# Kernel tuning notes

Hardware: AMD Instinct MI355X
Metric: run time of the kernel (lower is better)

Reference implementation:

```python
import jax, jax.numpy as jnp
import numpy as np

D_MODEL = 512
D_STATE = 16
D_CONV = 4
EXPAND = 2
D_INNER = EXPAND * D_MODEL  # 1024
DT_RANK = D_MODEL // 16     # 32 (ceil(512/16))
BATCH, SEQ = 8, 1024


def setup_inputs() -> dict:
    key = jax.random.key(0)
    ks = jax.random.split(key, 10)
    w = lambda i, shape, s=0.02: (jax.random.normal(ks[i], shape, jnp.float32) * s)
    return {
        "x": jax.random.normal(ks[0], (BATCH, SEQ, D_MODEL), jnp.float32),
        # Mamba params
        "W_in": w(1, (2 * D_INNER, D_MODEL)),            # in_proj (no bias)
        "conv_w": w(2, (D_INNER, D_CONV), 0.1),          # depthwise causal conv
        "conv_b": jnp.zeros((D_INNER,), jnp.float32),
        "W_x": w(3, (DT_RANK + 2 * D_STATE, D_INNER)),   # x_proj (no bias)
        "W_dt": w(4, (D_INNER, DT_RANK)),                # dt_proj
        "b_dt": jnp.full((D_INNER,), -4.6, jnp.float32), # -> softplus ~ 0.01
        "A_log": jnp.log(jnp.broadcast_to(
            jnp.arange(1, D_STATE + 1, dtype=jnp.float32), (D_INNER, D_STATE))),
        "D": jnp.ones((D_INNER,), jnp.float32),
        "W_out": w(5, (D_MODEL, D_INNER)),               # out_proj (no bias)
        # LayerNorm + head
        "ln_g": jnp.ones((D_MODEL,), jnp.float32),
        "ln_b": jnp.zeros((D_MODEL,), jnp.float32),
        "head_W": w(6, (D_MODEL, D_MODEL)),
        "head_b": jnp.zeros((D_MODEL,), jnp.float32),
    }


def reference(x, W_in, conv_w, conv_b, W_x, W_dt, b_dt, A_log, D, W_out,
              ln_g, ln_b, head_W, head_b):
    B, L, _ = x.shape
    # in_proj -> split into x branch and gate z
    xz = x @ W_in.T                               # (B, L, 2*D_INNER)
    xi, z = jnp.split(xz, 2, axis=-1)
    # causal depthwise conv1d over time (pad left d_conv-1), then SiLU
    xp = jnp.pad(xi, ((0, 0), (D_CONV - 1, 0), (0, 0)))
    xc = conv_b + sum(conv_w[:, k] * xp[:, k:k + L, :] for k in range(D_CONV))
    xc = jax.nn.silu(xc)                          # (B, L, D_INNER)
    # x_proj -> dt, B, C
    dbc = xc @ W_x.T
    dt = jax.nn.softplus(dbc[..., :DT_RANK] @ W_dt.T + b_dt)   # (B, L, D_INNER)
    Bm = dbc[..., DT_RANK:DT_RANK + D_STATE]                   # (B, L, D_STATE)
    Cm = dbc[..., DT_RANK + D_STATE:]                          # (B, L, D_STATE)
    A = -jnp.exp(A_log)                                        # (D_INNER, D_STATE)

    def step(h, ins):
        dt_t, B_t, C_t, u_t = ins                 # (B,Din) (B,Ds) (B,Ds) (B,Din)
        dA = jnp.exp(dt_t[:, :, None] * A)        # (B, Din, Ds)
        h = dA * h + (dt_t * u_t)[:, :, None] * B_t[:, None, :]
        y = jnp.einsum('bds,bs->bd', h, C_t)
        return h, y

    h0 = jnp.zeros((B, D_INNER, D_STATE), x.dtype)
    xs = (dt.transpose(1, 0, 2), Bm.transpose(1, 0, 2),
          Cm.transpose(1, 0, 2), xc.transpose(1, 0, 2))
    _, ys = jax.lax.scan(step, h0, xs)            # ys: (L, B, D_INNER)
    y = ys.transpose(1, 0, 2) + D * xc
    y = y * jax.nn.silu(z)
    out = y @ W_out.T                             # (B, L, D_MODEL)
    # LayerNorm is per-token, so norm the last token only (== LN(out)[:, -1])
    last = out[:, -1, :]
    mu = last.mean(-1, keepdims=True)
    var = ((last - mu) ** 2).mean(-1, keepdims=True)
    lastn = (last - mu) / jnp.sqrt(var + 1e-5) * ln_g + ln_b
    return lastn @ head_W.T + head_b              # (B, D_MODEL)
```

## Files before the change

kernel.cpp:

```cpp
#include <hip/hip_runtime.h>
#include <stdint.h>

#define B_   8
#define L_   1024
#define DM   512
#define DI   1024
#define DS   16
#define DTR  32
#define M_   (B_*L_)

typedef short v8s __attribute__((ext_vector_type(8)));
typedef short v4s __attribute__((ext_vector_type(4)));
typedef float v4f __attribute__((ext_vector_type(4)));

static __device__ __forceinline__ short f2bf(float f) {
  union { float f; uint32_t u; } v; v.f = f;
  uint32_t r = v.u + 0x7FFFu + ((v.u >> 16) & 1u);
  return (short)(r >> 16);
}
static __device__ __forceinline__ float bf2f(short s) {
  union { uint32_t u; float f; } v; v.u = ((uint32_t)(uint16_t)s) << 16; return v.f;
}
static __device__ __forceinline__ float silu_fast(float a) {
  return a * __builtin_amdgcn_rcpf(1.f + __expf(-a));
}
static __device__ __forceinline__ float wsum(float v) {
#pragma unroll
  for (int o = 32; o > 0; o >>= 1) v += __shfl_xor(v, o, 64);
  return v;
}
static __device__ __forceinline__ void gl_lds16(const short* g, short* l) {
  __builtin_amdgcn_global_load_lds(
      (const __attribute__((address_space(1))) void*)g,
      (__attribute__((address_space(3))) void*)l, 16, 0, 0);
}

__global__ __launch_bounds__(256) void k_prep(const float* __restrict__ x,
                                              const float* __restrict__ w_in,
                                              const float* __restrict__ w_x,
                                              const float* __restrict__ w_dt,
                                              const float* __restrict__ a_log,
                                              short* xb, short* wib, short* wxb, short* wdtb,
                                              float* Aneg, float* zlast) {
  if (blockIdx.x >= 4704) {
    int w = (int)(blockIdx.x - 4704) * 4 + (threadIdx.x >> 6);
    int l = threadIdx.x & 63;
    int b = w >> 10, j = w & 1023;
    const v4f* xr = (const v4f*)(x + ((size_t)(b * L_ + L_ - 1)) * DM);
    const v4f* wr = (const v4f*)(w_in + (size_t)(DI + j) * DM);
    float s = 0.f;
#pragma unroll
    for (int i = 0; i < 2; ++i) {
      v4f a = xr[l + 64 * i], c = wr[l + 64 * i];
      s += a[0]*c[0] + a[1]*c[1] + a[2]*c[2] + a[3]*c[3];
    }
    s = wsum(s);
    if (l == 0) zlast[b * DI + j] = s;
    return;
  }
  int idx = (blockIdx.x * 256 + threadIdx.x) * 4;
  const int n0 = M_ * DM, n1 = DI * DM, n2 = 48 * DI, n3 = DI * DTR, n4 = DI * DS;
  const float* src; short* dst;
  if (idx < n0)              { src = x + idx;    dst = xb + idx; }
  else if ((idx -= n0) < n1) { src = w_in + idx; dst = wib + idx; }
  else if ((idx -= n1) < n2) { src = w_x + idx;  dst = wxb + idx; }
  else if ((idx -= n2) < n3) { src = w_dt + idx; dst = wdtb + idx; }
  else if ((idx -= n3) < n4) {
    v4f v = *(const v4f*)(a_log + idx);
    v4f o;
#pragma unroll
    for (int i = 0; i < 4; ++i) o[i] = -__expf(v[i]);
    *(v4f*)(Aneg + idx) = o;
    return;
  }
  else return;
  v4f v = *(const v4f*)src;
  v4s o;
#pragma unroll
  for (int i = 0; i < 4; ++i) o[i] = f2bf(v[i]);
  *(v4s*)dst = o;
}

__global__ __launch_bounds__(256) void k_gemm_xi(const short* __restrict__ xb,
                                                 const short* __restrict__ wib,
                                                 short* __restrict__ xib) {
  __shared__ short sh[128 * 136];
  short* lA = sh;
  short* lB = sh + 128 * 64;
  int mb = blockIdx.x >> 3, nb = blockIdx.x & 7;
  int tid = threadIdx.x;
  int w = tid >> 6, l = tid & 63, lm = l & 15, q = l >> 4;
  int wm = (w >> 1) * 64, wn = (w & 1) * 64;

  v4f acc[4][4];
#pragma unroll
  for (int i = 0; i < 4; ++i)
#pragma unroll
    for (int j = 0; j < 4; ++j) acc[i][j] = (v4f){0,0,0,0};

  int srow_in_chunk = l >> 3;
  int sslot = l & 7;
  const short* Abase = xb  + (size_t)(mb * 128) * DM;
  const short* Bbase = wib + (size_t)(nb * 128) * DM;

  for (int k0 = 0; k0 < DM; k0 += 64) {
    if (k0) __syncthreads();
#pragma unroll
    for (int i = 0; i < 4; ++i) {
      int chunk = w * 4 + i;
      int row = chunk * 8 + srow_in_chunk;
      int c = sslot ^ (row & 7);
      gl_lds16(Abase + (size_t)row * DM + k0 + c * 8, lA + chunk * 512);
      gl_lds16(Bbase + (size_t)row * DM + k0 + c * 8, lB + chunk * 512);
    }
    __syncthreads();
#pragma unroll
    for (int kt = 0; kt < 2; ++kt) {
      v8s af[4], bf[4];
      int p = (kt * 4 + q) ^ (lm & 7);
#pragma unroll
      for (int t = 0; t < 4; ++t) {
        af[t] = *(const v8s*)(lA + (wm + t * 16 + lm) * 64 + p * 8);
        bf[t] = *(const v8s*)(lB + (wn + t * 16 + lm) * 64 + p * 8);
      }
#pragma unroll
      for (int i = 0; i < 4; ++i)
#pragma unroll
        for (int j = 0; j < 4; ++j)
          acc[i][j] = __builtin_amdgcn_mfma_f32_16x16x32_bf16(af[i], bf[j], acc[i][j], 0, 0, 0);
    }
  }
  __syncthreads();
#pragma unroll
  for (int i = 0; i < 4; ++i)
#pragma unroll
    for (int r = 0; r < 4; ++r) {
      int row = wm + i * 16 + q * 4 + r;
#pragma unroll
      for (int j = 0; j < 4; ++j)
        sh[row * 136 + wn + j * 16 + lm] = f2bf(acc[i][j][r]);
    }
  __syncthreads();
  int cc = tid & 15;
#pragma unroll
  for (int g = 0; g < 8; ++g) {
    int rr = (tid >> 4) + g * 16;
    v8s v = *(const v8s*)(sh + rr * 136 + cc * 8);
    *(v8s*)(xib + (size_t)(mb * 128 + rr) * DI + nb * 128 + cc * 8) = v;
  }
}

__global__ __launch_bounds__(256) void k_conv(const short* __restrict__ xib,
                                              const float* __restrict__ conv_w,
                                              const float* __restrict__ conv_b,
                                              short* __restrict__ xcb,
                                              float* __restrict__ xclast) {
  int bid = blockIdx.x;
  int b = bid >> 7, tc = bid & 127;
  int tid = threadIdx.x;
  int d8 = tid & 127, th = tid >> 7;
  int d = d8 * 8;
  int t0 = tc * 8 + th * 4;
  v4f cw[8];
  float cb[8];
#pragma unroll
  for (int i = 0; i < 8; ++i) {
    cw[i] = *(const v4f*)(conv_w + (d + i) * 4);
    cb[i] = conv_b[d + i];
  }
  float w0[8], w1[8], w2[8];
  const short* base = xib + (size_t)(b * L_) * DI + d;
  short* obase = xcb + (size_t)(b * L_) * DI + d;
#pragma unroll
  for (int i = 0; i < 8; ++i) { w0[i] = 0.f; w1[i] = 0.f; w2[i] = 0.f; }
  if (t0 >= 3) {
    v8s v0 = *(const v8s*)(base + (size_t)(t0 - 3) * DI);
    v8s v1 = *(const v8s*)(base + (size_t)(t0 - 2) * DI);
    v8s v2 = *(const v8s*)(base + (size_t)(t0 - 1) * DI);
#pragma unroll
    for (int i = 0; i < 8; ++i) { w0[i] = bf2f(v0[i]); w1[i] = bf2f(v1[i]); w2[i] = bf2f(v2[i]); }
  }
#pragma unroll
  for (int t = t0; t < t0 + 4; ++t) {
    v8s cur = *(const v8s*)(base + (size_t)t * DI);
    v8s ob;
#pragma unroll
    for (int i = 0; i < 8; ++i) {
      float xv = bf2f(cur[i]);
      float a = cb[i] + cw[i][0] * w0[i] + cw[i][1] * w1[i] + cw[i][2] * w2[i] + cw[i][3] * xv;
      float s = silu_fast(a);
      ob[i] = f2bf(s);
      if (t == L_ - 1) xclast[b * DI + d + i] = s;
      w0[i] = w1[i]; w1[i] = w2[i]; w2[i] = xv;
    }
    *(v8s*)(obase + (size_t)t * DI) = ob;
  }
}

__global__ __launch_bounds__(256) void k_dbcdt(const short* __restrict__ xcb,
                                               const short* __restrict__ wxb,
                                               const short* __restrict__ wdtb,
                                               const float* __restrict__ b_dt,
                                               float* __restrict__ Bmat,
                                               _Float16* __restrict__ dtO,
                                               float* __restrict__ csum2) {
  __shared__ float red[4 * 16 * 49];
  __shared__ short ta[16 * 32];
  int m = blockIdx.x;
  int tid = threadIdx.x, w = tid >> 6, l = tid & 63, lm = l & 15, q = l >> 4;
  v4f a0 = {0,0,0,0}, a1 = {0,0,0,0}, a2 = {0,0,0,0};
  const short* ap = xcb + (size_t)(m * 16 + lm) * DI + w * 256 + q * 8;
  const short* b0 = wxb + (size_t)lm * DI        + w * 256 + q * 8;
  const short* b1 = wxb + (size_t)(16 + lm) * DI + w * 256 + q * 8;
  const short* b2 = wxb + (size_t)(32 + lm) * DI + w * 256 + q * 8;
#pragma unroll
  for (int kk = 0; kk < 8; ++kk) {
    v8s a = *(const v8s*)(ap + kk * 32);
    a0 = __builtin_amdgcn_mfma_f32_16x16x32_bf16(a, *(const v8s*)(b0 + kk * 32), a0, 0, 0, 0);
    a1 = __builtin_amdgcn_mfma_f32_16x16x32_bf16(a, *(const v8s*)(b1 + kk * 32), a1, 0, 0, 0);
    a2 = __builtin_amdgcn_mfma_f32_16x16x32_bf16(a, *(const v8s*)(b2 + kk * 32), a2, 0, 0, 0);
  }
#pragma unroll
  for (int r = 0; r < 4; ++r) {
    int row = q * 4 + r;
    red[w * 784 + row * 49 + lm]      = a0[r];
    red[w * 784 + row * 49 + 16 + lm] = a1[r];
    red[w * 784 + row * 49 + 32 + lm] = a2[r];
  }
  __syncthreads();
  {
    int row = tid >> 4, c0 = tid & 15;
    int base = row * 49 + c0;
    float s0 = red[base] + red[784 + base] + red[1568 + base] + red[2352 + base];
    float s1 = red[base + 16] + red[784 + base + 16] + red[1568 + base + 16] + red[2352 + base + 16];
    float s2 = red[base + 32] + red[784 + base + 32] + red[1568 + base + 32] + red[2352 + base + 32];
    ta[row * 32 + c0]      = f2bf(s0);
    ta[row * 32 + 16 + c0] = f2bf(s1);
    Bmat[(size_t)(m * 16 + row) * DS + c0] = s2;
  }
  __syncthreads();
  v8s ad = *(const v8s*)(ta + lm * 32 + q * 8);
#pragma unroll 4
  for (int nn = 0; nn < 16; ++nn) {
    int nt = w * 16 + nn;
    v8s bb = *(const v8s*)(wdtb + (size_t)(nt * 16 + lm) * DTR + q * 8);
    v4f zz = {0,0,0,0};
    v4f dd = __builtin_amdgcn_mfma_f32_16x16x32_bf16(ad, bb, zz, 0, 0, 0);
    int col = nt * 16 + lm;
    float bd = b_dt[col];
    float s = 0.f;
#pragma unroll
    for (int r = 0; r < 4; ++r) {
      float v = dd[r] + bd;
      float sp = (v > 15.f) ? v : __logf(1.f + __expf(v));
      dtO[(size_t)(m * 16 + q * 4 + r) * DI + col] = (_Float16)sp;
      s += sp;
    }
    s += __shfl_xor(s, 16, 64);
    s += __shfl_xor(s, 32, 64);
    if (q == 0) csum2[(size_t)m * DI + col] = s;
  }
}

__global__ __launch_bounds__(256) void k_sufc(const float* __restrict__ csum2,
                                              const float* __restrict__ xclast,
                                              const float* __restrict__ w_x,
                                              float* __restrict__ SS,
                                              float* __restrict__ clast) {
  if (blockIdx.x < 32) {
    int b = blockIdx.x >> 2, dseg = blockIdx.x & 3;
    int d = dseg * 256 + threadIdx.x;
    float run = 0.f;
    for (int ch = 31; ch >= 0; --ch) {
      SS[(size_t)(b * 32 + ch) * DI + d] = run;
      run += csum2[(size_t)(b * 64 + 2 * ch + 1) * DI + d]
           + csum2[(size_t)(b * 64 + 2 * ch) * DI + d];
    }
  } else {
    int w2 = (int)(blockIdx.x - 32) * 4 + (threadIdx.x >> 6);
    int l = threadIdx.x & 63;
    int b = w2 >> 4, ss = w2 & 15;
    const v4f* xr = (const v4f*)(xclast + (size_t)b * DI);
    const v4f* wr = (const v4f*)(w_x + (size_t)(48 + ss) * DI);
    float s = 0.f;
#pragma unroll
    for (int i = 0; i < 4; ++i) {
      v4f a = xr[l + 64 * i], c = wr[l + 64 * i];
      s += a[0]*c[0] + a[1]*c[1] + a[2]*c[2] + a[3]*c[3];
    }
    s = wsum(s);
    if (l == 0) clast[b * 16 + ss] = s;
  }
}

__global__ __launch_bounds__(256) void k_scan(const _Float16* __restrict__ dt,
                                              const short* __restrict__ xcb,
                                              const float* __restrict__ Bmat,
                                              const float* __restrict__ SS,
                                              const float* __restrict__ Aneg,
                                              const float* __restrict__ clast,
                                              float* __restrict__ ypart) {
  __shared__ float lB[32 * 16];
  int bid = blockIdx.x;
  int b = bid >> 7, ch = (bid >> 2) & 31, dg = bid & 3;
  int tid = threadIdx.x;
  for (int i = tid; i < 32 * 16; i += 256)
    lB[i] = Bmat[(size_t)(b * L_ + ch * 32) * DS + i];
  __syncthreads();
  int d = dg * 256 + tid;
  float S = SS[(size_t)(b * 32 + ch) * DI + d];
  float As2[16];
#pragma unroll
  for (int s = 0; s < 16; ++s) As2[s] = Aneg[d * 16 + s] * 1.44269504f;
  float h[16];
#pragma unroll
  for (int s = 0; s < 16; ++s) h[s] = 0.f;
  const _Float16* dtp = dt + ((size_t)(b * L_ + ch * 32)) * DI + d;
  const short* xcp = xcb + ((size_t)(b * L_ + ch * 32)) * DI + d;
  for (int tl = 31; tl >= 0; --tl) {
    float dtv = (float)dtp[(size_t)tl * DI];
    float u   = bf2f(xcp[(size_t)tl * DI]);
    float c = dtv * u;
#pragma unroll
    for (int s = 0; s < 16; ++s)
      h[s] += __builtin_amdgcn_exp2f(As2[s] * S) * (c * lB[tl * 16 + s]);
    S += dtv;
  }
  float yp = 0.f;
#pragma unroll
  for (int s = 0; s < 16; ++s) yp += h[s] * clast[b * 16 + s];
  ypart[(size_t)(b * 32 + ch) * DI + d] = yp;
}

__global__ __launch_bounds__(256) void k_ylast(const float* __restrict__ ypart,
                                               const float* __restrict__ xclast,
                                               const float* __restrict__ Dp,
                                               const float* __restrict__ zlast,
                                               float* __restrict__ ylast) {
  int idx = blockIdx.x * 256 + threadIdx.x;
  int b = idx >> 10, d = idx & 1023;
  float acc = 0.f;
#pragma unroll 8
  for (int ch = 0; ch < 32; ++ch) acc += ypart[(size_t)(b * 32 + ch) * DI + d];
  float y = acc + Dp[d] * xclast[idx];
  ylast[idx] = y * silu_fast(zlast[idx]);
}

__global__ __launch_bounds__(256) void k_out(const float* __restrict__ ylast,
                                             const float* __restrict__ w_out,
                                             float* __restrict__ olast) {
  int w = blockIdx.x * 4 + (threadIdx.x >> 6);
  int l = threadIdx.x & 63;
  int b = w >> 9, i = w & 511;
  const v4f* yr = (const v4f*)(ylast + (size_t)b * DI);
  const v4f* wr = (const v4f*)(w_out + (size_t)i * DI);
  float s = 0.f;
#pragma unroll
  for (int k = 0; k < 4; ++k) {
    v4f a = yr[l + 64 * k], c = wr[l + 64 * k];
    s += a[0]*c[0] + a[1]*c[1] + a[2]*c[2] + a[3]*c[3];
  }
  s = wsum(s);
  if (l == 0) olast[b * DM + i] = s;
}

__global__ __launch_bounds__(256) void k_ln(const float* __restrict__ olast,
                                            const float* __restrict__ g,
                                            const float* __restrict__ be,
                                            float* __restrict__ lastn) {
  __shared__ float s1[256], s2[256];
  int b = blockIdx.x, tid = threadIdx.x;
  float v0 = olast[b * DM + tid], v1 = olast[b * DM + 256 + tid];
  s1[tid] = v0 + v1; s2[tid] = v0 * v0 + v1 * v1;
  __syncthreads();
  for (int o = 128; o > 0; o >>= 1) {
    if (tid < o) { s1[tid] += s1[tid + o]; s2[tid] += s2[tid + o]; }
    __syncthreads();
  }
  float mu = s1[0] / (float)DM;
  float var = s2[0] / (float)DM - mu * mu;
  float inv = 1.f / sqrtf(var + 1e-5f);
  lastn[b * DM + tid]       = (v0 - mu) * inv * g[tid]       + be[tid];
  lastn[b * DM + 256 + tid] = (v1 - mu) * inv * g[tid + 256] + be[tid + 256];
}

__global__ __launch_bounds__(256) void k_head(const float* __restrict__ lastn,
                                              const float* __restrict__ hw,
                                              const float* __restrict__ hb,
                                              float* __restrict__ out) {
  int w = blockIdx.x * 4 + (threadIdx.x >> 6);
  int l = threadIdx.x & 63;
  int b = w >> 9, o = w & 511;
  const v4f* xr = (const v4f*)(lastn + (size_t)b * DM);
  const v4f* wr = (const v4f*)(hw + (size_t)o * DM);
  float s = 0.f;
#pragma unroll
  for (int k = 0; k < 2; ++k) {
    v4f a = xr[l + 64 * k], c = wr[l + 64 * k];
    s += a[0]*c[0] + a[1]*c[1] + a[2]*c[2] + a[3]*c[3];
  }
  s = wsum(s);
  if (l == 0) out[b * DM + o] = s + hb[o];
}

extern "C" void kernel_launch(void* const* d_in, const int* in_sizes, int n_in,
                              void* d_out, int out_size, void* d_ws, size_t ws_size,
                              hipStream_t stream) {
  const float* x      = (const float*)d_in[0];
  const float* w_in   = (const float*)d_in[1];
  const float* conv_w = (const float*)d_in[2];
  const float* conv_b = (const float*)d_in[3];
  const float* w_x    = (const float*)d_in[4];
  const float* w_dt   = (const float*)d_in[5];
  const float* b_dt   = (const float*)d_in[6];
  const float* a_log  = (const float*)d_in[7];
  const float* Dp     = (const float*)d_in[8];
  const float* w_out  = (const float*)d_in[9];
  const float* ln_g   = (const float*)d_in[10];
  const float* ln_b   = (const float*)d_in[11];
  const float* head_W = (const float*)d_in[12];
  const float* head_b = (const float*)d_in[13];
  float* out = (float*)d_out;

  char* ws = (char*)d_ws;
  size_t off = 0;
  auto alloc = [&](size_t bytes) { void* p = ws + off; off += (bytes + 255) & ~(size_t)255; return p; };
  short* xb     = (short*)alloc((size_t)M_*DM*2);
  short* wib    = (short*)alloc((size_t)DI*DM*2);
  short* wxb    = (short*)alloc((size_t)48*DI*2);
  short* wdtb   = (short*)alloc((size_t)DI*DTR*2);
  float* Aneg   = (float*)alloc((size_t)DI*DS*4);
  short* xib    = (short*)alloc((size_t)M_*DI*2);
  short* xcb    = (short*)alloc((size_t)M_*DI*2);
  _Float16* dt  = (_Float16*)alloc((size_t)M_*DI*2);
  float* Bmat   = (float*)alloc((size_t)M_*DS*4);
  float* csum2  = (float*)alloc((size_t)512*DI*4);
  float* SS     = (float*)alloc((size_t)B_*32*DI*4);
  float* ypart  = (float*)alloc((size_t)B_*32*DI*4);
  float* zlast  = (float*)alloc((size_t)B_*DI*4);
  float* clast  = (float*)alloc((size_t)B_*DS*4);
  float* xclast = (float*)alloc((size_t)B_*DI*4);
  float* ylast  = (float*)alloc((size_t)B_*DI*4);
  float* olast  = (float*)alloc((size_t)B_*DM*4);
  float* lastn  = (float*)alloc((size_t)B_*DM*4);

  k_prep<<<6752, 256, 0, stream>>>(x, w_in, w_x, w_dt, a_log, xb, wib, wxb, wdtb, Aneg, zlast);
  k_gemm_xi<<<512, 256, 0, stream>>>(xb, wib, xib);
  k_conv<<<1024, 256, 0, stream>>>(xib, conv_w, conv_b, xcb, xclast);
  k_dbcdt<<<512, 256, 0, stream>>>(xcb, wxb, wdtb, b_dt, Bmat, dt, csum2);
  k_sufc<<<64, 256, 0, stream>>>(csum2, xclast, w_x, SS, clast);
  k_scan<<<1024, 256, 0, stream>>>(dt, xcb, Bmat, SS, Aneg, clast, ypart);
  k_ylast<<<32, 256, 0, stream>>>(ypart, xclast, Dp, zlast, ylast);
  k_out<<<1024, 256, 0, stream>>>(ylast, w_out, olast);
  k_ln<<<8, 256, 0, stream>>>(olast, ln_g, ln_b, lastn);
  k_head<<<1024, 256, 0, stream>>>(lastn, head_W, head_b, out);
}
```

Measured before the change: 179.7 us.

## Fuse causal conv into in_proj GEMM epilogue and collapse tail kernels

```diff
diff --git a/kernel.cpp b/kernel.cpp
--- a/kernel.cpp
+++ b/kernel.cpp
@@ -41,7 +41,14 @@
                                               const float* __restrict__ w_dt,
                                               const float* __restrict__ a_log,
                                               short* xb, short* wib, short* wxb, short* wdtb,
-                                              float* Aneg, float* zlast) {
+                                              float* Aneg, float* zlast,
+                                              float* yraw, float* stat) {
+  if (blockIdx.x >= 6752) {
+    int i = (int)(blockIdx.x - 6752) * 256 + threadIdx.x;
+    if (i < 2048)      *(v4f*)(yraw + (size_t)i * 4) = (v4f){0,0,0,0};
+    else if (i < 2052) *(v4f*)(stat + (size_t)(i - 2048) * 4) = (v4f){0,0,0,0};
+    return;
+  }
   if (blockIdx.x >= 4704) {
     int w = (int)(blockIdx.x - 4704) * 4 + (threadIdx.x >> 6);
     int l = threadIdx.x & 63;
@@ -81,9 +88,14 @@
   *(v4s*)dst = o;
 }
 
-__global__ __launch_bounds__(256) void k_gemm_xi(const short* __restrict__ xb,
-                                                 const short* __restrict__ wib,
-                                                 short* __restrict__ xib) {
+__global__ __launch_bounds__(256) void k_gemmconv(const short* __restrict__ xb,
+                                                  const short* __restrict__ wib,
+                                                  const float* __restrict__ conv_w,
+                                                  const float* __restrict__ conv_b,
+                                                  short* __restrict__ xcb,
+                                                  short* __restrict__ haloF,
+                                                  short* __restrict__ haloL,
+                                                  float* __restrict__ xclast) {
   __shared__ short sh[128 * 136];
   short* lA = sh;
   short* lB = sh + 128 * 64;
@@ -142,59 +154,72 @@
     }
   __syncthreads();
   int cc = tid & 15;
+  int ch0 = nb * 128 + cc * 8;
+  v4f cw[8]; float cb[8];
+#pragma unroll
+  for (int i = 0; i < 8; ++i) {
+    cw[i] = *(const v4f*)(conv_w + (ch0 + i) * 4);
+    cb[i] = conv_b[ch0 + i];
+  }
+  int bB = mb >> 3;
+  bool top = (mb & 7) == 7;
 #pragma unroll
   for (int g = 0; g < 8; ++g) {
     int rr = (tid >> 4) + g * 16;
-    v8s v = *(const v8s*)(sh + rr * 136 + cc * 8);
-    *(v8s*)(xib + (size_t)(mb * 128 + rr) * DI + nb * 128 + cc * 8) = v;
-  }
-}
-
-__global__ __launch_bounds__(256) void k_conv(const short* __restrict__ xib,
-                                              const float* __restrict__ conv_w,
-                                              const float* __restrict__ conv_b,
-                                              short* __restrict__ xcb,
-                                              float* __restrict__ xclast) {
-  int bid = blockIdx.x;
-  int b = bid >> 7, tc = bid & 127;
-  int tid = threadIdx.x;
-  int d8 = tid & 127, th = tid >> 7;
-  int d = d8 * 8;
-  int t0 = tc * 8 + th * 4;
-  v4f cw[8];
-  float cb[8];
+    if (rr < 3) {
+      *(v8s*)(haloF + ((size_t)(mb * 3 + rr) << 10) + ch0) =
+          *(const v8s*)(sh + rr * 136 + cc * 8);
+    } else {
+      if (rr >= 125)
+        *(v8s*)(haloL + ((size_t)(mb * 3 + rr - 125) << 10) + ch0) =
+            *(const v8s*)(sh + rr * 136 + cc * 8);
+      v8s x0 = *(const v8s*)(sh + (rr - 3) * 136 + cc * 8);
+      v8s x1 = *(const v8s*)(sh + (rr - 2) * 136 + cc * 8);
+      v8s x2 = *(const v8s*)(sh + (rr - 1) * 136 + cc * 8);
+      v8s x3 = *(const v8s*)(sh + rr * 136 + cc * 8);
+      v8s ob;
+#pragma unroll
+      for (int i = 0; i < 8; ++i) {
+        float a = cb[i] + cw[i][0] * bf2f(x0[i]) + cw[i][1] * bf2f(x1[i])
+                        + cw[i][2] * bf2f(x2[i]) + cw[i][3] * bf2f(x3[i]);
+        float s = silu_fast(a);
+        ob[i] = f2bf(s);
+        if (top && rr == 127) xclast[bB * DI + ch0 + i] = s;
+      }
+      *(v8s*)(xcb + (size_t)(mb * 128 + rr) * DI + ch0) = ob;
+    }
+  }
+}
+
+__global__ __launch_bounds__(256) void k_convfix(const short* __restrict__ haloF,
+                                                 const short* __restrict__ haloL,
+                                                 const float* __restrict__ conv_w,
+                                                 const float* __restrict__ conv_b,
+                                                 short* __restrict__ xcb) {
+  int gid = blockIdx.x * 256 + threadIdx.x;
+  int cc = gid & 127;
+  int r  = (gid >> 7) % 3;
+  int mb = gid / 384;
+  int ch0 = cc * 8;
+  float xin[4][8];
+#pragma unroll
+  for (int k = 0; k < 4; ++k) {
+    int p = r - 3 + k;
+    v8s v = 0;
+    if (p >= 0)            v = *(const v8s*)(haloF + ((size_t)(mb * 3 + p) << 10) + ch0);
+    else if (mb & 7)       v = *(const v8s*)(haloL + ((size_t)((mb - 1) * 3 + 3 + p) << 10) + ch0);
+#pragma unroll
+    for (int i = 0; i < 8; ++i) xin[k][i] = bf2f(v[i]);
+  }
+  v8s ob;
 #pragma unroll
   for (int i = 0; i < 8; ++i) {
-    cw[i] = *(const v4f*)(conv_w + (d + i) * 4);
-    cb[i] = conv_b[d + i];
-  }
-  float w0[8], w1[8], w2[8];
-  const short* base = xib + (size_t)(b * L_) * DI + d;
-  short* obase = xcb + (size_t)(b * L_) * DI + d;
-#pragma unroll
-  for (int i = 0; i < 8; ++i) { w0[i] = 0.f; w1[i] = 0.f; w2[i] = 0.f; }
-  if (t0 >= 3) {
-    v8s v0 = *(const v8s*)(base + (size_t)(t0 - 3) * DI);
-    v8s v1 = *(const v8s*)(base + (size_t)(t0 - 2) * DI);
-    v8s v2 = *(const v8s*)(base + (size_t)(t0 - 1) * DI);
-#pragma unroll
-    for (int i = 0; i < 8; ++i) { w0[i] = bf2f(v0[i]); w1[i] = bf2f(v1[i]); w2[i] = bf2f(v2[i]); }
-  }
-#pragma unroll
-  for (int t = t0; t < t0 + 4; ++t) {
-    v8s cur = *(const v8s*)(base + (size_t)t * DI);
-    v8s ob;
-#pragma unroll
-    for (int i = 0; i < 8; ++i) {
-      float xv = bf2f(cur[i]);
-      float a = cb[i] + cw[i][0] * w0[i] + cw[i][1] * w1[i] + cw[i][2] * w2[i] + cw[i][3] * xv;
-      float s = silu_fast(a);
-      ob[i] = f2bf(s);
-      if (t == L_ - 1) xclast[b * DI + d + i] = s;
-      w0[i] = w1[i]; w1[i] = w2[i]; w2[i] = xv;
-    }
-    *(v8s*)(obase + (size_t)t * DI) = ob;
-  }
+    v4f cw = *(const v4f*)(conv_w + (ch0 + i) * 4);
+    float a = conv_b[ch0 + i] + cw[0]*xin[0][i] + cw[1]*xin[1][i]
+                              + cw[2]*xin[2][i] + cw[3]*xin[3][i];
+    ob[i] = f2bf(silu_fast(a));
+  }
+  *(v8s*)(xcb + (size_t)(mb * 128 + r) * DI + ch0) = ob;
 }
 
 __global__ __launch_bounds__(256) void k_dbcdt(const short* __restrict__ xcb,
@@ -299,7 +324,7 @@
                                               const float* __restrict__ SS,
                                               const float* __restrict__ Aneg,
                                               const float* __restrict__ clast,
-                                              float* __restrict__ ypart) {
+                                              float* __restrict__ yraw) {
   __shared__ float lB[32 * 16];
   int bid = blockIdx.x;
   int b = bid >> 7, ch = (bid >> 2) & 31, dg = bid & 3;
@@ -329,75 +354,67 @@
   float yp = 0.f;
 #pragma unroll
   for (int s = 0; s < 16; ++s) yp += h[s] * clast[b * 16 + s];
-  ypart[(size_t)(b * 32 + ch) * DI + d] = yp;
-}
-
-__global__ __launch_bounds__(256) void k_ylast(const float* __restrict__ ypart,
-                                               const float* __restrict__ xclast,
-                                               const float* __restrict__ Dp,
-                                               const float* __restrict__ zlast,
-                                               float* __restrict__ ylast) {
-  int idx = blockIdx.x * 256 + threadIdx.x;
-  int b = idx >> 10, d = idx & 1023;
-  float acc = 0.f;
-#pragma unroll 8
-  for (int ch = 0; ch < 32; ++ch) acc += ypart[(size_t)(b * 32 + ch) * DI + d];
-  float y = acc + Dp[d] * xclast[idx];
-  ylast[idx] = y * silu_fast(zlast[idx]);
-}
-
-__global__ __launch_bounds__(256) void k_out(const float* __restrict__ ylast,
+  atomicAdd(yraw + (size_t)b * DI + d, yp);
+}
+
+__global__ __launch_bounds__(256) void k_out(const float* __restrict__ yraw,
+                                             const float* __restrict__ xclast,
+                                             const float* __restrict__ Dp,
+                                             const float* __restrict__ zlast,
                                              const float* __restrict__ w_out,
-                                             float* __restrict__ olast) {
+                                             float* __restrict__ olast,
+                                             float* __restrict__ stat) {
   int w = blockIdx.x * 4 + (threadIdx.x >> 6);
   int l = threadIdx.x & 63;
   int b = w >> 9, i = w & 511;
-  const v4f* yr = (const v4f*)(ylast + (size_t)b * DI);
+  const v4f* yr = (const v4f*)(yraw + (size_t)b * DI);
+  const v4f* xc = (const v4f*)(xclast + (size_t)b * DI);
+  const v4f* zz = (const v4f*)(zlast + (size_t)b * DI);
+  const v4f* dv = (const v4f*)Dp;
   const v4f* wr = (const v4f*)(w_out + (size_t)i * DI);
   float s = 0.f;
 #pragma unroll
   for (int k = 0; k < 4; ++k) {
-    v4f a = yr[l + 64 * k], c = wr[l + 64 * k];
-    s += a[0]*c[0] + a[1]*c[1] + a[2]*c[2] + a[3]*c[3];
+    v4f a = yr[l + 64 * k], x = xc[l + 64 * k], z = zz[l + 64 * k];
+    v4f dd = dv[l + 64 * k], c = wr[l + 64 * k];
+#pragma unroll
+    for (int j = 0; j < 4; ++j) {
+      float ye = (a[j] + dd[j] * x[j]) * silu_fast(z[j]);
+      s += ye * c[j];
+    }
   }
   s = wsum(s);
-  if (l == 0) olast[b * DM + i] = s;
-}
-
-__global__ __launch_bounds__(256) void k_ln(const float* __restrict__ olast,
-                                            const float* __restrict__ g,
-                                            const float* __restrict__ be,
-                                            float* __restrict__ lastn) {
-  __shared__ float s1[256], s2[256];
-  int b = blockIdx.x, tid = threadIdx.x;
-  float v0 = olast[b * DM + tid], v1 = olast[b * DM + 256 + tid];
-  s1[tid] = v0 + v1; s2[tid] = v0 * v0 + v1 * v1;
-  __syncthreads();
-  for (int o = 128; o > 0; o >>= 1) {
-    if (tid < o) { s1[tid] += s1[tid + o]; s2[tid] += s2[tid + o]; }
-    __syncthreads();
-  }
-  float mu = s1[0] / (float)DM;
-  float var = s2[0] / (float)DM - mu * mu;
-  float inv = 1.f / sqrtf(var + 1e-5f);
-  lastn[b * DM + tid]       = (v0 - mu) * inv * g[tid]       + be[tid];
-  lastn[b * DM + 256 + tid] = (v1 - mu) * inv * g[tid + 256] + be[tid + 256];
-}
-
-__global__ __launch_bounds__(256) void k_head(const float* __restrict__ lastn,
+  if (l == 0) {
+    olast[b * DM + i] = s;
+    atomicAdd(&stat[b * 2], s);
+    atomicAdd(&stat[b * 2 + 1], s * s);
+  }
+}
+
+__global__ __launch_bounds__(256) void k_head(const float* __restrict__ olast,
+                                              const float* __restrict__ stat,
+                                              const float* __restrict__ g,
+                                              const float* __restrict__ be,
                                               const float* __restrict__ hw,
                                               const float* __restrict__ hb,
                                               float* __restrict__ out) {
   int w = blockIdx.x * 4 + (threadIdx.x >> 6);
   int l = threadIdx.x & 63;
   int b = w >> 9, o = w & 511;
-  const v4f* xr = (const v4f*)(lastn + (size_t)b * DM);
+  float mu  = stat[b * 2]     * (1.f / (float)DM);
+  float ex2 = stat[b * 2 + 1] * (1.f / (float)DM);
+  float inv = __frsqrt_rn(ex2 - mu * mu + 1e-5f);
+  const v4f* xr = (const v4f*)(olast + (size_t)b * DM);
+  const v4f* gg = (const v4f*)g;
+  const v4f* bb = (const v4f*)be;
   const v4f* wr = (const v4f*)(hw + (size_t)o * DM);
   float s = 0.f;
 #pragma unroll
   for (int k = 0; k < 2; ++k) {
-    v4f a = xr[l + 64 * k], c = wr[l + 64 * k];
-    s += a[0]*c[0] + a[1]*c[1] + a[2]*c[2] + a[3]*c[3];
+    v4f a = xr[l + 64 * k], gv = gg[l + 64 * k], bv = bb[l + 64 * k], c = wr[l + 64 * k];
+#pragma unroll
+    for (int j = 0; j < 4; ++j)
+      s += ((a[j] - mu) * inv * gv[j] + bv[j]) * c[j];
   }
   s = wsum(s);
   if (l == 0) out[b * DM + o] = s + hb[o];
@@ -430,28 +447,27 @@
   short* wxb    = (short*)alloc((size_t)48*DI*2);
   short* wdtb   = (short*)alloc((size_t)DI*DTR*2);
   float* Aneg   = (float*)alloc((size_t)DI*DS*4);
-  short* xib    = (short*)alloc((size_t)M_*DI*2);
   short* xcb    = (short*)alloc((size_t)M_*DI*2);
   _Float16* dt  = (_Float16*)alloc((size_t)M_*DI*2);
   float* Bmat   = (float*)alloc((size_t)M_*DS*4);
   float* csum2  = (float*)alloc((size_t)512*DI*4);
   float* SS     = (float*)alloc((size_t)B_*32*DI*4);
-  float* ypart  = (float*)alloc((size_t)B_*32*DI*4);
   float* zlast  = (float*)alloc((size_t)B_*DI*4);
   float* clast  = (float*)alloc((size_t)B_*DS*4);
   float* xclast = (float*)alloc((size_t)B_*DI*4);
-  float* ylast  = (float*)alloc((size_t)B_*DI*4);
+  float* yraw   = (float*)alloc((size_t)B_*DI*4);
   float* olast  = (float*)alloc((size_t)B_*DM*4);
-  float* lastn  = (float*)alloc((size_t)B_*DM*4);
-
-  k_prep<<<6752, 256, 0, stream>>>(x, w_in, w_x, w_dt, a_log, xb, wib, wxb, wdtb, Aneg, zlast);
-  k_gemm_xi<<<512, 256, 0, stream>>>(xb, wib, xib);
-  k_conv<<<1024, 256, 0, stream>>>(xib, conv_w, conv_b, xcb, xclast);
+  float* stat   = (float*)alloc((size_t)16*4);
+  short* haloF  = (short*)alloc((size_t)64*3*DI*2);
+  short* haloL  = (short*)alloc((size_t)64*3*DI*2);
+
+  k_prep<<<6761, 256, 0, stream>>>(x, w_in, w_x, w_dt, a_log, xb, wib, wxb, wdtb,
+                                   Aneg, zlast, yraw, stat);
+  k_gemmconv<<<512, 256, 0, stream>>>(xb, wib, conv_w, conv_b, xcb, haloF, haloL, xclast);
+  k_convfix<<<96, 256, 0, stream>>>(haloF, haloL, conv_w, conv_b, xcb);
   k_dbcdt<<<512, 256, 0, stream>>>(xcb, wxb, wdtb, b_dt, Bmat, dt, csum2);
   k_sufc<<<64, 256, 0, stream>>>(csum2, xclast, w_x, SS, clast);
-  k_scan<<<1024, 256, 0, stream>>>(dt, xcb, Bmat, SS, Aneg, clast, ypart);
-  k_ylast<<<32, 256, 0, stream>>>(ypart, xclast, Dp, zlast, ylast);
-  k_out<<<1024, 256, 0, stream>>>(ylast, w_out, olast);
-  k_ln<<<8, 256, 0, stream>>>(olast, ln_g, ln_b, lastn);
-  k_head<<<1024, 256, 0, stream>>>(lastn, head_W, head_b, out);
-}
+  k_scan<<<1024, 256, 0, stream>>>(dt, xcb, Bmat, SS, Aneg, clast, yraw);
+  k_out<<<1024, 256, 0, stream>>>(yraw, xclast, Dp, zlast, w_out, olast, stat);
+  k_head<<<1024, 256, 0, stream>>>(olast, stat, ln_g, ln_b, head_W, head_b, out);
+}
```

Measured after the change: 279.4 us. 1.55x slower.
